# Kernel tuning notes

Hardware: AMD Instinct MI355X
Metric: run time of the kernel (lower is better)

The kernel has to match this reference:

```python
import jax, jax.numpy as jnp
import numpy as np

B, N, L, D, H, DH = 1, 512, 256, 256, 8, 32  # batch, n_seqs, length, d_msa, heads, d_hidden
EPS = 1e-5


def setup_inputs() -> dict:
    key = jax.random.key(0)
    ks = jax.random.split(key, 3)
    msa = jax.random.normal(ks[0], (B, N, L, D), dtype=jnp.float32)
    # xavier-uniform-ish scale for (H*DH, D) linear weights
    lim = float(np.sqrt(6.0 / (D + H * DH)))
    Wq = jax.random.uniform(ks[1], (H * DH, D), minval=-lim, maxval=lim, dtype=jnp.float32)
    Wk = jax.random.uniform(ks[2], (H * DH, D), minval=-lim, maxval=lim, dtype=jnp.float32)
    return {
        "msa": msa,
        "Wq": Wq,
        "bq": jnp.zeros((H * DH,), jnp.float32),
        "Wk": Wk,
        "bk": jnp.zeros((H * DH,), jnp.float32),
        "ln_gamma": jnp.ones((D,), jnp.float32),
        "ln_beta": jnp.zeros((D,), jnp.float32),
        "stride": 0,
    }


def reference(msa, Wq, bq, Wk, bk, ln_gamma, ln_beta, stride):
    # stride only controls chunking in the original (no math effect); ignored.
    def ln(x):
        m = jnp.mean(x, axis=-1, keepdims=True)
        v = jnp.mean((x - m) ** 2, axis=-1, keepdims=True)
        return (x - m) * jax.lax.rsqrt(v + EPS) * ln_gamma + ln_beta

    scale = 1.0 / np.sqrt(DH)
    b, n, l = msa.shape[:3]
    # query from target (first) sequence: (B, L, H, DH)
    q = (ln(msa[:, 0]) @ Wq.T + bq).reshape(b, l, H, DH) * scale
    # keys from all sequences: (B, N, L, H, DH)
    k = (ln(msa) @ Wk.T + bk).reshape(b, n, l, H, DH)
    # attention logits over the sequence axis N: (B, N, L, H)
    logits = jnp.einsum("blhd,bnlhd->bnlh", q, k)
    attn = jax.nn.softmax(logits, axis=1)
    # dropout is identity in eval mode
    return attn[..., None]  # (B, N, L, H, 1)
```

## Files before the change

### kernel.cpp

```cpp
#include <hip/hip_runtime.h>
#include <hip/hip_bf16.h>
#include <cstdint>

#define LL 256
#define NN 512
#define DD 256
#define HH 8
#define EPSF 1e-5f
#define WGS 264

typedef __attribute__((ext_vector_type(8))) __bf16 bf16x8;
typedef __attribute__((ext_vector_type(4))) float f32x4;

static __device__ __forceinline__ void load_group(
    const float* __restrict__ msa, int l, int wave, int col, int kb, int g,
    float4 (&buf)[16])
{
    const float* rp = msa + ((size_t)(g * 128 + (wave << 4) + col) * LL + l) * DD + (kb << 3);
    #pragma unroll
    for (int ks = 0; ks < 8; ++ks) {
        buf[2 * ks]     = *(const float4*)(rp + ks * 32);
        buf[2 * ks + 1] = *(const float4*)(rp + ks * 32 + 4);
    }
}

static __device__ __forceinline__ void compute_group(
    const float4 (&buf)[16], const bf16x8 (&bfr)[8], f32x4& hacc, f32x4& gacc)
{
    #pragma unroll
    for (int ks = 0; ks < 8; ++ks) {
        float4 u = buf[2 * ks], v = buf[2 * ks + 1];
        bf16x8 a;
        a[0] = (__bf16)u.x; a[1] = (__bf16)u.y; a[2] = (__bf16)u.z; a[3] = (__bf16)u.w;
        a[4] = (__bf16)v.x; a[5] = (__bf16)v.y; a[6] = (__bf16)v.z; a[7] = (__bf16)v.w;
        hacc = __builtin_amdgcn_mfma_f32_16x16x32_bf16(a, bfr[ks], hacc, 0, 0, 0);
        gacc = __builtin_amdgcn_mfma_f32_16x16x32_bf16(a, a,       gacc, 0, 0, 0);
    }
}

static __device__ __forceinline__ void store_group(
    int g, int wave, int col, int kb, const f32x4& hacc, const f32x4& gacc,
    float* logits, float* sS, float* sQ)
{
    const int nb = g * 128 + (wave << 4);
    #pragma unroll
    for (int i = 0; i < 4; ++i) {
        int n = nb + (kb << 2) + i;
        if (col < HH)       logits[col * NN + n] = hacc[i];
        else if (col == HH) sS[n] = hacc[i];
    }
    if (kb == (col >> 2)) sQ[nb + col] = gacc[col & 3];
}

__global__
__attribute__((amdgpu_flat_work_group_size(512, 512), amdgpu_waves_per_eu(2, 2)))
void k_fused(
    const float* __restrict__ msa, const float* __restrict__ Wq,
    const float* __restrict__ bq, const float* __restrict__ Wk,
    const float* __restrict__ gamma, const float* __restrict__ beta,
    float* __restrict__ out)
{
    const int l = blockIdx.x;
    const int tid = threadIdx.x, wave = tid >> 6, lane = tid & 63;
    const int col = lane & 15, kb = lane >> 4;

    __shared__ __align__(16) float logits[HH * NN];
    __shared__ __align__(16) float sS[NN];
    __shared__ __align__(16) float sQ[NN];
    __shared__ __align__(16) __bf16 WgL[16 * WGS];
    __shared__ float lnx[DD];
    __shared__ float qv[DD];
    __shared__ float red[8];
    __shared__ float stats[16];
    __shared__ float Gs[HH];

    float4 A[16], B[16];
    load_group(msa, l, wave, col, kb, 0, A);
    load_group(msa, l, wave, col, kb, 1, B);

    {
        float x0 = (tid < DD) ? msa[(size_t)l * DD + tid] : 0.f;
        float s = x0, ss = x0 * x0;
        #pragma unroll
        for (int m = 32; m >= 1; m >>= 1) { s += __shfl_xor(s, m); ss += __shfl_xor(ss, m); }
        if (tid < DD && lane == 0) { red[wave * 2] = s; red[wave * 2 + 1] = ss; }
        __syncthreads();
        if (tid < DD) {
            float sm = red[0] + red[2] + red[4] + red[6];
            float sq = red[1] + red[3] + red[5] + red[7];
            float mean = sm * (1.f / DD);
            float var  = sq * (1.f / DD) - mean * mean;
            float rs   = rsqrtf(var + EPSF);
            lnx[tid] = (x0 - mean) * rs * gamma[tid] + beta[tid];
        }
        __syncthreads();
        const int r = tid & 255, hf = tid >> 8;
        float acc = 0.f;
        {
            const float4* wr = (const float4*)(Wq + (size_t)r * DD) + hf * 32;
            const float* lx = lnx + hf * 128;
            #pragma unroll 4
            for (int j = 0; j < 32; ++j) {
                float4 w4 = wr[j];
                acc += lx[4*j] * w4.x + lx[4*j+1] * w4.y + lx[4*j+2] * w4.z + lx[4*j+3] * w4.w;
            }
        }
        if (hf == 0) qv[r] = acc;
        __syncthreads();
        if (hf == 1) qv[r] = (qv[r] + acc + bq[r]) * 0.17677669529663687f;
        __syncthreads();
        const int c = tid & 255, h0 = (tid >> 8) * 4;
        const float gm = gamma[c];
        #pragma unroll
        for (int hi = 0; hi < 4; ++hi) {
            int h = h0 + hi;
            float a = 0.f;
            const float* wk = Wk + ((size_t)h * 32) * DD + c;
            #pragma unroll 8
            for (int d = 0; d < 32; ++d)
                a += qv[h * 32 + d] * wk[(size_t)d * DD];
            WgL[h * WGS + c] = (__bf16)(gm * a);
        }
        if (tid < DD) {
            WgL[8 * WGS + tid] = (__bf16)1.0f;
        } else {
            const int c2 = tid - 256;
            #pragma unroll
            for (int h = 9; h < 16; ++h) WgL[h * WGS + c2] = (__bf16)0.0f;
        }
        __syncthreads();
        if (wave < HH) {
            float gsum = 0.f;
            #pragma unroll
            for (int i = 0; i < 4; ++i) gsum += (float)WgL[wave * WGS + lane * 4 + i];
            #pragma unroll
            for (int m = 32; m >= 1; m >>= 1) gsum += __shfl_xor(gsum, m);
            if (lane == 0) Gs[wave] = gsum;
        }
        __syncthreads();
    }

    bf16x8 bfr[8];
    #pragma unroll
    for (int ks = 0; ks < 8; ++ks)
        bfr[ks] = *(const bf16x8*)&WgL[col * WGS + ks * 32 + kb * 8];

    const f32x4 z = {0.f, 0.f, 0.f, 0.f};
    {
        f32x4 ha = z, ga = z;
        compute_group(A, bfr, ha, ga);
        load_group(msa, l, wave, col, kb, 2, A);
        store_group(0, wave, col, kb, ha, ga, logits, sS, sQ);
    }
    {
        f32x4 ha = z, ga = z;
        compute_group(B, bfr, ha, ga);
        load_group(msa, l, wave, col, kb, 3, B);
        store_group(1, wave, col, kb, ha, ga, logits, sS, sQ);
    }
    {
        f32x4 ha = z, ga = z;
        compute_group(A, bfr, ha, ga);
        store_group(2, wave, col, kb, ha, ga, logits, sS, sQ);
    }
    {
        f32x4 ha = z, ga = z;
        compute_group(B, bfr, ha, ga);
        store_group(3, wave, col, kb, ha, ga, logits, sS, sQ);
    }
    __syncthreads();

    {
        const int h = wave;
        const float Gh = Gs[h];
        const float* lp = logits + h * NN;
        float4 ra = ((const float4*)lp)[lane * 2];
        float4 rb = ((const float4*)lp)[lane * 2 + 1];
        float4 sa = ((const float4*)sS)[lane * 2];
        float4 sb = ((const float4*)sS)[lane * 2 + 1];
        float4 qa = ((const float4*)sQ)[lane * 2];
        float4 qb = ((const float4*)sQ)[lane * 2 + 1];
        float raw[8] = {ra.x, ra.y, ra.z, ra.w, rb.x, rb.y, rb.z, rb.w};
        float sv[8]  = {sa.x, sa.y, sa.z, sa.w, sb.x, sb.y, sb.z, sb.w};
        float qv2[8] = {qa.x, qa.y, qa.z, qa.w, qb.x, qb.y, qb.z, qb.w};
        float adj[8];
        #pragma unroll
        for (int i = 0; i < 8; ++i) {
            float mean = sv[i] * (1.f / DD);
            float var  = qv2[i] * (1.f / DD) - mean * mean;
            float rs   = rsqrtf(var + EPSF);
            adj[i] = rs * (raw[i] - mean * Gh);
        }
        float mx = adj[0];
        #pragma unroll
        for (int i = 1; i < 8; ++i) mx = fmaxf(mx, adj[i]);
        #pragma unroll
        for (int m = 32; m >= 1; m >>= 1) mx = fmaxf(mx, __shfl_xor(mx, m));
        float sm = 0.f;
        #pragma unroll
        for (int i = 0; i < 8; ++i) sm += __expf(adj[i] - mx);
        #pragma unroll
        for (int m = 32; m >= 1; m >>= 1) sm += __shfl_xor(sm, m);
        if (lane == 0) { stats[wave] = mx; stats[8 + wave] = 1.f / sm; }
    }
    __syncthreads();

    {
        const int n = tid;
        float s = sS[n], q2 = sQ[n];
        float mean = s * (1.f / DD);
        float var  = q2 * (1.f / DD) - mean * mean;
        float rs   = rsqrtf(var + EPSF);
        float o[8];
        #pragma unroll
        for (int h = 0; h < HH; ++h) {
            float adj = rs * (logits[h * NN + n] - mean * Gs[h]);
            o[h] = __expf(adj - stats[h]) * stats[8 + h];
        }
        float* op = out + (size_t)n * LL * HH + (size_t)l * HH;
        float4 p0 = {o[0], o[1], o[2], o[3]};
        float4 p1 = {o[4], o[5], o[6], o[7]};
        *(float4*)(op)     = p0;
        *(float4*)(op + 4) = p1;
    }
}

extern "C" void kernel_launch(void* const* d_in, const int* in_sizes, int n_in,
                              void* d_out, int out_size, void* d_ws, size_t ws_size,
                              hipStream_t stream) {
    (void)in_sizes; (void)n_in; (void)out_size; (void)d_ws; (void)ws_size;
    const float* msa   = (const float*)d_in[0];
    const float* Wq    = (const float*)d_in[1];
    const float* bq    = (const float*)d_in[2];
    const float* Wk    = (const float*)d_in[3];
    const float* gamma = (const float*)d_in[5];
    const float* beta  = (const float*)d_in[6];
    k_fused<<<dim3(LL), dim3(512), 0, stream>>>(msa, Wq, bq, Wk, gamma, beta, (float*)d_out);
}
```

Baseline: 42.93 us.

## Double workgroup to 1024 threads and use lightweight LDS-only barriers

The workgroup grows from 8 to 16 waves. Each wave now processes two 16-row groups of the MSA column with a single register buffer instead of four groups with double buffering. The Wq matvec is split four ways across threads and the Wk projection two heads per thread. All __syncthreads are replaced by a barrier that waits only on LDS counters, so outstanding global loads are not drained at each sync. The aim is more waves per CU for latency hiding and cheaper barriers, at the cost of less per-wave prefetch overlap and more register pressure under the 1024-thread launch bound.

```diff
diff --git a/kernel.cpp b/kernel.cpp
--- a/kernel.cpp
+++ b/kernel.cpp
@@ -12,11 +12,17 @@
 typedef __attribute__((ext_vector_type(8))) __bf16 bf16x8;
 typedef __attribute__((ext_vector_type(4))) float f32x4;
 
+static __device__ __forceinline__ void lb_sync() {
+    __builtin_amdgcn_sched_barrier(0);
+    asm volatile("s_waitcnt lgkmcnt(0)" ::: "memory");
+    __builtin_amdgcn_s_barrier();
+    __builtin_amdgcn_sched_barrier(0);
+}
+
 static __device__ __forceinline__ void load_group(
-    const float* __restrict__ msa, int l, int wave, int col, int kb, int g,
-    float4 (&buf)[16])
-{
-    const float* rp = msa + ((size_t)(g * 128 + (wave << 4) + col) * LL + l) * DD + (kb << 3);
+    const float* __restrict__ msa, int l, int row0, int col, int kb, float4 (&buf)[16])
+{
+    const float* rp = msa + ((size_t)(row0 + col) * LL + l) * DD + (kb << 3);
     #pragma unroll
     for (int ks = 0; ks < 8; ++ks) {
         buf[2 * ks]     = *(const float4*)(rp + ks * 32);
@@ -39,22 +45,19 @@
 }
 
 static __device__ __forceinline__ void store_group(
-    int g, int wave, int col, int kb, const f32x4& hacc, const f32x4& gacc,
+    int nloc0, int col, int kb, const f32x4& hacc, const f32x4& gacc,
     float* logits, float* sS, float* sQ)
 {
-    const int nb = g * 128 + (wave << 4);
     #pragma unroll
     for (int i = 0; i < 4; ++i) {
-        int n = nb + (kb << 2) + i;
+        int n = nloc0 + (kb << 2) + i;
         if (col < HH)       logits[col * NN + n] = hacc[i];
         else if (col == HH) sS[n] = hacc[i];
     }
-    if (kb == (col >> 2)) sQ[nb + col] = gacc[col & 3];
-}
-
-__global__
-__attribute__((amdgpu_flat_work_group_size(512, 512), amdgpu_waves_per_eu(2, 2)))
-void k_fused(
+    if (kb == (col >> 2)) sQ[nloc0 + col] = gacc[col & 3];
+}
+
+__global__ __launch_bounds__(1024, 4) void k_fused(
     const float* __restrict__ msa, const float* __restrict__ Wq,
     const float* __restrict__ bq, const float* __restrict__ Wk,
     const float* __restrict__ gamma, const float* __restrict__ beta,
@@ -68,67 +71,69 @@
     __shared__ __align__(16) float sS[NN];
     __shared__ __align__(16) float sQ[NN];
     __shared__ __align__(16) __bf16 WgL[16 * WGS];
+    __shared__ __align__(16) float qpart[4][264];
     __shared__ float lnx[DD];
     __shared__ float qv[DD];
-    __shared__ float red[8];
+    __shared__ float red8[8];
     __shared__ float stats[16];
     __shared__ float Gs[HH];
 
-    float4 A[16], B[16];
-    load_group(msa, l, wave, col, kb, 0, A);
-    load_group(msa, l, wave, col, kb, 1, B);
+    float4 A[16];
+    load_group(msa, l, wave * 16, col, kb, A);
 
     {
         float x0 = (tid < DD) ? msa[(size_t)l * DD + tid] : 0.f;
         float s = x0, ss = x0 * x0;
         #pragma unroll
         for (int m = 32; m >= 1; m >>= 1) { s += __shfl_xor(s, m); ss += __shfl_xor(ss, m); }
-        if (tid < DD && lane == 0) { red[wave * 2] = s; red[wave * 2 + 1] = ss; }
-        __syncthreads();
+        if (tid < DD && lane == 0) { red8[wave * 2] = s; red8[wave * 2 + 1] = ss; }
+        lb_sync();
         if (tid < DD) {
-            float sm = red[0] + red[2] + red[4] + red[6];
-            float sq = red[1] + red[3] + red[5] + red[7];
+            float sm = red8[0] + red8[2] + red8[4] + red8[6];
+            float sq = red8[1] + red8[3] + red8[5] + red8[7];
             float mean = sm * (1.f / DD);
             float var  = sq * (1.f / DD) - mean * mean;
             float rs   = rsqrtf(var + EPSF);
             lnx[tid] = (x0 - mean) * rs * gamma[tid] + beta[tid];
         }
-        __syncthreads();
-        const int r = tid & 255, hf = tid >> 8;
-        float acc = 0.f;
+        lb_sync();
         {
-            const float4* wr = (const float4*)(Wq + (size_t)r * DD) + hf * 32;
-            const float* lx = lnx + hf * 128;
+            const int r = tid & 255, qtr = tid >> 8;
+            const float4* wr = (const float4*)(Wq + (size_t)r * DD) + qtr * 16;
+            const float* lx = lnx + qtr * 64;
+            float acc = 0.f;
             #pragma unroll 4
-            for (int j = 0; j < 32; ++j) {
+            for (int j = 0; j < 16; ++j) {
                 float4 w4 = wr[j];
                 acc += lx[4*j] * w4.x + lx[4*j+1] * w4.y + lx[4*j+2] * w4.z + lx[4*j+3] * w4.w;
             }
-        }
-        if (hf == 0) qv[r] = acc;
-        __syncthreads();
-        if (hf == 1) qv[r] = (qv[r] + acc + bq[r]) * 0.17677669529663687f;
-        __syncthreads();
-        const int c = tid & 255, h0 = (tid >> 8) * 4;
-        const float gm = gamma[c];
-        #pragma unroll
-        for (int hi = 0; hi < 4; ++hi) {
-            int h = h0 + hi;
-            float a = 0.f;
-            const float* wk = Wk + ((size_t)h * 32) * DD + c;
-            #pragma unroll 8
-            for (int d = 0; d < 32; ++d)
-                a += qv[h * 32 + d] * wk[(size_t)d * DD];
-            WgL[h * WGS + c] = (__bf16)(gm * a);
+            qpart[qtr][r] = acc;
+        }
+        lb_sync();
+        if (tid < DD)
+            qv[tid] = (qpart[0][tid] + qpart[1][tid] + qpart[2][tid] + qpart[3][tid]
+                       + bq[tid]) * 0.17677669529663687f;
+        lb_sync();
+        {
+            const int c = tid & 255, hb = tid >> 8;
+            const float gm = gamma[c];
+            #pragma unroll
+            for (int hi = 0; hi < 2; ++hi) {
+                int h = hb + hi * 4;
+                float a = 0.f;
+                const float* wk = Wk + ((size_t)h * 32) * DD + c;
+                #pragma unroll 8
+                for (int d = 0; d < 32; ++d)
+                    a += qv[h * 32 + d] * wk[(size_t)d * DD];
+                WgL[h * WGS + c] = (__bf16)(gm * a);
+            }
         }
         if (tid < DD) {
             WgL[8 * WGS + tid] = (__bf16)1.0f;
-        } else {
-            const int c2 = tid - 256;
-            #pragma unroll
-            for (int h = 9; h < 16; ++h) WgL[h * WGS + c2] = (__bf16)0.0f;
-        }
-        __syncthreads();
+            #pragma unroll
+            for (int h = 9; h < 16; ++h) WgL[h * WGS + tid] = (__bf16)0.0f;
+        }
+        lb_sync();
         if (wave < HH) {
             float gsum = 0.f;
             #pragma unroll
@@ -137,7 +142,7 @@
             for (int m = 32; m >= 1; m >>= 1) gsum += __shfl_xor(gsum, m);
             if (lane == 0) Gs[wave] = gsum;
         }
-        __syncthreads();
+        lb_sync();
     }
 
     bf16x8 bfr[8];
@@ -149,28 +154,17 @@
     {
         f32x4 ha = z, ga = z;
         compute_group(A, bfr, ha, ga);
-        load_group(msa, l, wave, col, kb, 2, A);
-        store_group(0, wave, col, kb, ha, ga, logits, sS, sQ);
-    }
-    {
-        f32x4 ha = z, ga = z;
-        compute_group(B, bfr, ha, ga);
-        load_group(msa, l, wave, col, kb, 3, B);
-        store_group(1, wave, col, kb, ha, ga, logits, sS, sQ);
-    }
+        store_group(wave * 16, col, kb, ha, ga, logits, sS, sQ);
+    }
+    load_group(msa, l, 256 + wave * 16, col, kb, A);
     {
         f32x4 ha = z, ga = z;
         compute_group(A, bfr, ha, ga);
-        store_group(2, wave, col, kb, ha, ga, logits, sS, sQ);
-    }
-    {
-        f32x4 ha = z, ga = z;
-        compute_group(B, bfr, ha, ga);
-        store_group(3, wave, col, kb, ha, ga, logits, sS, sQ);
-    }
-    __syncthreads();
-
-    {
+        store_group(256 + wave * 16, col, kb, ha, ga, logits, sS, sQ);
+    }
+    lb_sync();
+
+    if (wave < HH) {
         const int h = wave;
         const float Gh = Gs[h];
         const float* lp = logits + h * NN;
@@ -203,9 +197,9 @@
         for (int m = 32; m >= 1; m >>= 1) sm += __shfl_xor(sm, m);
         if (lane == 0) { stats[wave] = mx; stats[8 + wave] = 1.f / sm; }
     }
-    __syncthreads();
-
-    {
+    lb_sync();
+
+    if (tid < NN) {
         const int n = tid;
         float s = sS[n], q2 = sQ[n];
         float mean = s * (1.f / DD);
@@ -235,5 +229,5 @@
     const float* Wk    = (const float*)d_in[3];
     const float* gamma = (const float*)d_in[5];
     const float* beta  = (const float*)d_in[6];
-    k_fused<<<dim3(LL), dim3(512), 0, stream>>>(msa, Wq, bq, Wk, gamma, beta, (float*)d_out);
-}
+    k_fused<<<dim3(LL), dim3(1024), 0, stream>>>(msa, Wq, bq, Wk, gamma, beta, (float*)d_out);
+}
```

New measurement: 41.07 us. 1.05x faster.
